# Kernel tuning notes

Measured on AMD Instinct MI355X. Metric: run time of the kernel, lower is better.

## Reference

```python
import jax, jax.numpy as jnp
import numpy as np

# ---- module config (mirrors arch_args / init_kwargs) ----
W_BITS_PER_SLICE = 4      # slice_init=True -> weights quantized with STE to w_bits_per_slice
A_BITS = 8                # activation quantization bits
A_BITS_PER_STREAM = 8
VMAX = 1.0
GON_HW, GOFF_HW = 1.0, 1e-3   # weight_to_diff_conductance is called with Gon=1, Goff=1/1000 (hardcoded)
ADC_PREC = 8
ADC_STEP = 1e-3           # adc_static_step
NUM_SUBARRAYS = 9
SUB_SIZE = 256            # subarray_size; 256*3*3 / 256 = 9 even chunks
K, STRIDE, PAD = 3, 1, 1


def ste_quantize(x, bits):
    # Symmetric uniform quantizer with straight-through estimator (STE_Quantize).
    n = float(2 ** bits - 1)
    s = jnp.max(jnp.abs(x)) + 1e-12
    q = jnp.round(x / s * n) / n * s
    return x + jax.lax.stop_gradient(q - x)


def adc_quantize(I):
    # Nbit_ADC: static-step uniform ADC, signed (adc_pos_only=False), deterministic
    # rounding (adc_stoch_round=False), STE backward, no custom loss.
    half = 2 ** (ADC_PREC - 1)
    q = jnp.clip(jnp.round(I / ADC_STEP), -half, half - 1) * ADC_STEP
    return I + jax.lax.stop_gradient(q - I)


def setup_inputs():
    key = jax.random.key(0)
    k1, k2 = jax.random.split(key)
    x = jax.random.normal(k1, (32, 256, 32, 32), jnp.float32)
    fan_in = 256 * K * K
    w = jax.random.normal(k2, (256, 256, K, K), jnp.float32) * np.sqrt(2.0 / fan_in)  # kaiming_normal
    return {"inputs": x, "weight": w}


def reference(inputs, weight):
    B = inputs.shape[0]
    O = weight.shape[0]

    # forward(): quantize activations (a_bits) and weights (w_bits_per_slice, slice_init path)
    qa = ste_quantize(inputs, A_BITS)
    qw = ste_quantize(weight, W_BITS_PER_SLICE)

    # F.unfold -> [B, C*k*k, L], channel-major patch ordering (matches torch)
    patches = jax.lax.conv_general_dilated_patches(
        qa, (K, K), (STRIDE, STRIDE), ((PAD, PAD), (PAD, PAD)))
    Hp, Wp = patches.shape[2], patches.shape[3]
    L = Hp * Wp
    V = patches.reshape(B, NUM_SUBARRAYS, SUB_SIZE, L) * (VMAX / A_BITS_PER_STREAM)

    # Differential conductances: G_pos - G_neg. The dummy columns (both filled with
    # Goff) cancel exactly in I_pos - I_neg, so the net current per subarray is a
    # single contraction against qw * (Gon - Goff) / Nstates_slice.
    nstates = float(2 ** W_BITS_PER_SLICE - 1)
    Gd = qw.reshape(O, NUM_SUBARRAYS, SUB_SIZE) * ((GON_HW - GOFF_HW) / nstates)

    # per-subarray crossbar currents: [B, n_sub, O, L]
    I = jnp.einsum('bgfl,ogf->bgol', V, Gd)

    # shared ADC applied to each subarray output, then accumulate over subarrays
    accum = adc_quantize(I).sum(axis=1)  # [B, O, L]
    a_loss = jnp.float32(0.0)            # adc_custom_loss=False

    # F.fold with (1,1) kernel onto sqrt(L) x sqrt(L) grid == reshape
    result = accum.reshape(B, O, Hp, Wp)
    return (result, a_loss)
```

## Files before the change

### kernel.cpp

```cpp
#include <hip/hip_runtime.h>
#include <stdint.h>

typedef unsigned short u16;
typedef __attribute__((ext_vector_type(8))) short short8;
typedef __attribute__((ext_vector_type(4))) float floatx4;

#define NB 32
#define NC 256
#define NH 32
#define NW 32
#define NO 256
#define NPIX (NH*NW)
#define KPIX 9
#define NG 9
#define RUN 32
#define GK (NG*RUN)
#define KTOT (NG*GK)
#define PADH 34
#define PADSP (PADH*PADH)
#define QA_BSTRIDE (PADSP*NC)

#define AS1 __attribute__((address_space(1)))
#define AS3 __attribute__((address_space(3)))

__global__ void fused_pre(const float4* __restrict__ x4, int nx4,
                          const float4* __restrict__ w4, int nw4,
                          float* __restrict__ pmax, u16* __restrict__ qa) {
  int bid = blockIdx.x;
  if (bid >= 1088) {
    int zb = bid - 1088;
    int b = zb / 9;
    int rem = (zb % 9) * 256 + threadIdx.x;
    if (rem >= 2112) return;
    int pb = rem >> 4, c16 = rem & 15;
    int y, x;
    if (pb < 68) { y = (pb >= 34) ? 33 : 0; x = pb % 34; }
    else { int q = pb - 68; y = 1 + (q >> 1); x = (q & 1) ? 33 : 0; }
    uint4 z; z.x = z.y = z.z = z.w = 0u;
    *(uint4*)(qa + ((size_t)(b * PADH + y) * PADH + x) * NC + c16 * 16) = z;
    return;
  }
  const float4* p; int n4; int nb, b0;
  if (bid < 1024) { p = x4; n4 = nx4; nb = 1024; b0 = bid; }
  else            { p = w4; n4 = nw4; nb = 64;   b0 = bid - 1024; }
  float m = 0.f;
  for (int i = b0 * blockDim.x + threadIdx.x; i < n4; i += nb * blockDim.x) {
    float4 v = p[i];
    m = fmaxf(m, fmaxf(fmaxf(fabsf(v.x), fabsf(v.y)), fmaxf(fabsf(v.z), fabsf(v.w))));
  }
#pragma unroll
  for (int off = 32; off > 0; off >>= 1)
    m = fmaxf(m, __shfl_down(m, off, 64));
  __shared__ float sm[4];
  int lane = threadIdx.x & 63, wv = threadIdx.x >> 6;
  if (lane == 0) sm[wv] = m;
  __syncthreads();
  if (threadIdx.x == 0)
    pmax[bid] = fmaxf(fmaxf(sm[0], sm[1]), fmaxf(sm[2], sm[3]));
}

__device__ inline void reduce_pmax(const float* pmax, int tid, int nthreads,
                                   float* sred, float& mx_out, float& mw_out) {
  const float4* pf4 = (const float4*)pmax;
  float mx = 0.f, mw = 0.f;
  for (int t = tid; t < 256; t += nthreads) {
    float4 v = pf4[t];
    mx = fmaxf(mx, fmaxf(fmaxf(v.x, v.y), fmaxf(v.z, v.w)));
  }
  if (tid < 16) {
    float4 v = pf4[256 + tid];
    mw = fmaxf(fmaxf(v.x, v.y), fmaxf(v.z, v.w));
  }
#pragma unroll
  for (int off = 32; off > 0; off >>= 1) {
    mx = fmaxf(mx, __shfl_down(mx, off, 64));
    mw = fmaxf(mw, __shfl_down(mw, off, 64));
  }
  int lane = tid & 63, wv = tid >> 6, nw = nthreads >> 6;
  if (lane == 0) { sred[wv] = mx; sred[8 + wv] = mw; }
  __syncthreads();
  mx = sred[0]; mw = sred[8];
  for (int i = 1; i < nw; i++) { mx = fmaxf(mx, sred[i]); mw = fmaxf(mw, sred[8 + i]); }
  mx_out = mx; mw_out = mw;
}

__global__ void fused_quant(const float* __restrict__ x, const float* __restrict__ w,
                            const float* __restrict__ pmax,
                            u16* __restrict__ qa, u16* __restrict__ wq,
                            float* __restrict__ lossp) {
  __shared__ float sred[16];
  float mx, mw;
  reduce_pmax(pmax, threadIdx.x, 256, sred, mx, mw);
  int bid = blockIdx.x, tid = threadIdx.x;
  if (bid < 1024) {
    __shared__ u16 ts[32][264];
    double s = (double)mx + 1e-12;
    double inv = 255.0 / s;
    int b = bid >> 5, y = bid & 31;
    const float4* x4 = (const float4*)x;
    int xc = tid & 7, crow = tid >> 3;
#pragma unroll
    for (int it = 0; it < 8; it++) {
      int c = crow + 32 * it;
      float4 v = x4[((size_t)(b * NC + c) * NH + y) * 8 + xc];
      float q0 = (float)rint((double)v.x * inv);
      float q1 = (float)rint((double)v.y * inv);
      float q2 = (float)rint((double)v.z * inv);
      float q3 = (float)rint((double)v.w * inv);
      ts[xc * 4 + 0][c] = (u16)(__float_as_uint(q0) >> 16);
      ts[xc * 4 + 1][c] = (u16)(__float_as_uint(q1) >> 16);
      ts[xc * 4 + 2][c] = (u16)(__float_as_uint(q2) >> 16);
      ts[xc * 4 + 3][c] = (u16)(__float_as_uint(q3) >> 16);
    }
    __syncthreads();
    int xx = tid >> 3, qwl = tid & 7;
    u16* orow = qa + ((size_t)(b * PADH + y + 1) * PADH + (xx + 1)) * NC;
#pragma unroll
    for (int it = 0; it < 4; it++) {
      int qw = qwl + 8 * it;
      *(uint4*)(orow + qw * 8) = *(const uint4*)&ts[xx][qw * 8];
    }
    return;
  }
  double s = (double)mw + 1e-12;
  double inv = 15.0 / s;
  int idx = (bid - 1024) * 256 + tid;
  if (idx == 0) *lossp = 0.0f;
  int o = idx / KTOT, kk = idx % KTOT;
  int g = kk / GK, rem = kk % GK;
  int r = rem / RUN, j = rem % RUN;
  int clo = (256 * g - r + 8) / 9;
  int chi = (256 * (g + 1) - r + 8) / 9; if (chi > NC) chi = NC;
  int cst = clo & ~3;
  int c = cst + j;
  float val = 0.f;
  if (c >= clo && c < chi) {
    float wv = w[((size_t)o * NC + c) * KPIX + r];
    val = (float)rint((double)wv * inv);
  }
  wq[idx] = (u16)(__float_as_uint(val) >> 16);
}

__global__ __launch_bounds__(256, 2) void gemm_adc(const u16* __restrict__ qa,
                                                   const u16* __restrict__ wq,
                                                   const float* __restrict__ pmax,
                                                   float* __restrict__ out) {
  __shared__ u16 lA[3 * 128 * RUN];
  __shared__ u16 lB[3 * 128 * RUN];
  __shared__ float sred[16];
  const int tid = threadIdx.x;
  float mx, mw;
  reduce_pmax(pmax, tid, 256, sred, mx, mw);

  const int mblk = blockIdx.x, nblk = blockIdx.y;
  const int b = mblk >> 3;
  const int p0 = (mblk & 7) * 128;
  const int n0 = nblk * 128;
  const int lane = tid & 63, wv = tid >> 6;
  const int wm = (wv & 1) * 64, wn = (wv >> 1) * 64;
  const int fm = lane & 15, fq = lane >> 4;
  const int swz = (fq + ((fm >> 1) & 3)) & 3;

  double sa = (double)mx + 1e-12;
  double sw = (double)mw + 1e-12;
  double Sstep = sa * sw * 0.999 / 459.0;

  const int r0 = tid >> 2;
  const int jsrc = ((tid & 3) - ((tid >> 3) & 3)) & 3;
  const u16* AbH[2]; const u16* BbH[2];
#pragma unroll
  for (int h = 0; h < 2; h++) {
    int row = r0 + 64 * h;
    int p = p0 + row;
    AbH[h] = qa + (size_t)b * QA_BSTRIDE
             + (((p >> 5) + 1) * PADH + ((p & 31) + 1)) * NC + jsrc * 8;
    BbH[h] = wq + (size_t)(n0 + row) * KTOT + jsrc * 8;
  }

  floatx4 acc[4][4];
  float tot[4][4][4];
#pragma unroll
  for (int mi = 0; mi < 4; mi++)
#pragma unroll
    for (int ni = 0; ni < 4; ni++)
#pragma unroll
      for (int rr = 0; rr < 4; rr++) { acc[mi][ni][rr] = 0.f; tot[mi][ni][rr] = 0.f; }

#pragma unroll 1
  for (int g = 0; g < NG; g++) {
#pragma unroll 1
    for (int rc = 0; rc < 3; rc++) {
      int offA[3], kb[3];
#pragma unroll
      for (int ri = 0; ri < 3; ri++) {
        int r = rc * 3 + ri;
        int cst = ((256 * g - r + 8) / 9) & ~3;
        offA[ri] = ((rc - 1) * PADH + (ri - 1)) * NC + cst;
        kb[ri] = g * GK + r * RUN;
      }
#pragma unroll
      for (int i = 0; i < 6; i++)
        __builtin_amdgcn_global_load_lds(
            (const AS1 void*)(AbH[i & 1] + offA[i >> 1]),
            (AS3 void*)&lA[(tid + 256 * i) * 8], 16, 0, 0);
#pragma unroll
      for (int i = 0; i < 6; i++)
        __builtin_amdgcn_global_load_lds(
            (const AS1 void*)(BbH[i & 1] + kb[i >> 1]),
            (AS3 void*)&lB[(tid + 256 * i) * 8], 16, 0, 0);
      __syncthreads();
#pragma unroll
      for (int ri = 0; ri < 3; ri++) {
        short8 afr[4], bfr[4];
#pragma unroll
        for (int mi = 0; mi < 4; mi++)
          afr[mi] = *(const short8*)&lA[ri * 4096 + (wm + mi * 16 + fm) * RUN + swz * 8];
#pragma unroll
        for (int ni = 0; ni < 4; ni++)
          bfr[ni] = *(const short8*)&lB[ri * 4096 + (wn + ni * 16 + fm) * RUN + swz * 8];
#pragma unroll
        for (int mi = 0; mi < 4; mi++)
#pragma unroll
          for (int ni = 0; ni < 4; ni++)
            acc[mi][ni] = __builtin_amdgcn_mfma_f32_16x16x32_bf16(afr[mi], bfr[ni], acc[mi][ni], 0, 0, 0);
      }
      __syncthreads();
    }
#pragma unroll
    for (int mi = 0; mi < 4; mi++)
#pragma unroll
      for (int ni = 0; ni < 4; ni++)
#pragma unroll
        for (int rr = 0; rr < 4; rr++) {
          double d = (double)acc[mi][ni][rr] * Sstep;
          float tf = (float)rint(d);
          tf = fminf(fmaxf(tf, -128.f), 127.f);
          tot[mi][ni][rr] += tf;
          acc[mi][ni][rr] = 0.f;
        }
  }
#pragma unroll
  for (int mi = 0; mi < 4; mi++)
#pragma unroll
    for (int ni = 0; ni < 4; ni++) {
      int o = n0 + wn + ni * 16 + fm;
      int p = p0 + wm + mi * 16 + fq * 4;
      float4 o4;
      o4.x = tot[mi][ni][0] * 1e-3f;
      o4.y = tot[mi][ni][1] * 1e-3f;
      o4.z = tot[mi][ni][2] * 1e-3f;
      o4.w = tot[mi][ni][3] * 1e-3f;
      *(float4*)(out + ((size_t)(b * NO + o)) * NPIX + p) = o4;
    }
}

extern "C" void kernel_launch(void* const* d_in, const int* in_sizes, int n_in,
                              void* d_out, int out_size, void* d_ws, size_t ws_size,
                              hipStream_t stream) {
  const float* x = (const float*)d_in[0];
  const float* w = (const float*)d_in[1];
  float* out = (float*)d_out;

  float* pmax = (float*)d_ws;
  u16* qa = (u16*)((char*)d_ws + 8192);
  u16* wq = (u16*)((char*)d_ws + 8192 + 18939904 + 8192);

  fused_pre<<<1376, 256, 0, stream>>>((const float4*)x, (NB * NC * NH * NW) / 4,
                                      (const float4*)w, (NO * NC * KPIX) / 4,
                                      pmax, qa);
  fused_quant<<<1024 + 2592, 256, 0, stream>>>(x, w, pmax, qa, wq, out + (out_size - 1));
  gemm_adc<<<dim3(256, 2), 256, 0, stream>>>(qa, wq, pmax, out);
}
```

Baseline: 158.6 us.

## Double-buffer LDS loads in gemm_adc and enlarge block tile to 256x128

The GEMM+ADC kernel now uses 512 threads per block with a 256-pixel by 128-output tile, so each B tile is shared across twice as many rows. Global-to-LDS loads are double-buffered: the next stage is issued before computing the current one, with a partial vmcnt wait and raw barriers replacing __syncthreads, and MFMA sections run at raised wave priority. This aims to hide load latency and cut redundant weight traffic. The cost is a larger LDS footprint (about 144KB per block), which may limit occupancy to one block per CU, and only 256 blocks in the grid.

```diff
diff --git a/kernel.cpp b/kernel.cpp
--- a/kernel.cpp
+++ b/kernel.cpp
@@ -141,23 +141,23 @@
   wq[idx] = (u16)(__float_as_uint(val) >> 16);
 }
 
-__global__ __launch_bounds__(256, 2) void gemm_adc(const u16* __restrict__ qa,
+__global__ __launch_bounds__(512, 2) void gemm_adc(const u16* __restrict__ qa,
                                                    const u16* __restrict__ wq,
                                                    const float* __restrict__ pmax,
                                                    float* __restrict__ out) {
-  __shared__ u16 lA[3 * 128 * RUN];
-  __shared__ u16 lB[3 * 128 * RUN];
+  __shared__ u16 lA[2 * 3 * 256 * RUN];
+  __shared__ u16 lB[2 * 3 * 128 * RUN];
   __shared__ float sred[16];
   const int tid = threadIdx.x;
   float mx, mw;
-  reduce_pmax(pmax, tid, 256, sred, mx, mw);
+  reduce_pmax(pmax, tid, 512, sred, mx, mw);
 
   const int mblk = blockIdx.x, nblk = blockIdx.y;
-  const int b = mblk >> 3;
-  const int p0 = (mblk & 7) * 128;
+  const int b = mblk >> 2;
+  const int p0 = (mblk & 3) * 256;
   const int n0 = nblk * 128;
   const int lane = tid & 63, wv = tid >> 6;
-  const int wm = (wv & 1) * 64, wn = (wv >> 1) * 64;
+  const int wm = (wv & 3) * 64, wn = (wv >> 2) * 64;
   const int fm = lane & 15, fq = lane >> 4;
   const int swz = (fq + ((fm >> 1) & 3)) & 3;
 
@@ -167,15 +167,14 @@
 
   const int r0 = tid >> 2;
   const int jsrc = ((tid & 3) - ((tid >> 3) & 3)) & 3;
-  const u16* AbH[2]; const u16* BbH[2];
+  const u16* AbH[2];
 #pragma unroll
   for (int h = 0; h < 2; h++) {
-    int row = r0 + 64 * h;
-    int p = p0 + row;
+    int p = p0 + r0 + 128 * h;
     AbH[h] = qa + (size_t)b * QA_BSTRIDE
              + (((p >> 5) + 1) * PADH + ((p & 31) + 1)) * NC + jsrc * 8;
-    BbH[h] = wq + (size_t)(n0 + row) * KTOT + jsrc * 8;
-  }
+  }
+  const u16* Bb = wq + (size_t)(n0 + r0) * KTOT + jsrc * 8;
 
   floatx4 acc[4][4];
   float tot[4][4][4];
@@ -186,46 +185,28 @@
 #pragma unroll
       for (int rr = 0; rr < 4; rr++) { acc[mi][ni][rr] = 0.f; tot[mi][ni][rr] = 0.f; }
 
-#pragma unroll 1
-  for (int g = 0; g < NG; g++) {
-#pragma unroll 1
-    for (int rc = 0; rc < 3; rc++) {
-      int offA[3], kb[3];
-#pragma unroll
-      for (int ri = 0; ri < 3; ri++) {
-        int r = rc * 3 + ri;
-        int cst = ((256 * g - r + 8) / 9) & ~3;
-        offA[ri] = ((rc - 1) * PADH + (ri - 1)) * NC + cst;
-        kb[ri] = g * GK + r * RUN;
-      }
-#pragma unroll
-      for (int i = 0; i < 6; i++)
-        __builtin_amdgcn_global_load_lds(
-            (const AS1 void*)(AbH[i & 1] + offA[i >> 1]),
-            (AS3 void*)&lA[(tid + 256 * i) * 8], 16, 0, 0);
-#pragma unroll
-      for (int i = 0; i < 6; i++)
-        __builtin_amdgcn_global_load_lds(
-            (const AS1 void*)(BbH[i & 1] + kb[i >> 1]),
-            (AS3 void*)&lB[(tid + 256 * i) * 8], 16, 0, 0);
-      __syncthreads();
-#pragma unroll
-      for (int ri = 0; ri < 3; ri++) {
-        short8 afr[4], bfr[4];
-#pragma unroll
-        for (int mi = 0; mi < 4; mi++)
-          afr[mi] = *(const short8*)&lA[ri * 4096 + (wm + mi * 16 + fm) * RUN + swz * 8];
-#pragma unroll
-        for (int ni = 0; ni < 4; ni++)
-          bfr[ni] = *(const short8*)&lB[ri * 4096 + (wn + ni * 16 + fm) * RUN + swz * 8];
-#pragma unroll
-        for (int mi = 0; mi < 4; mi++)
-#pragma unroll
-          for (int ni = 0; ni < 4; ni++)
-            acc[mi][ni] = __builtin_amdgcn_mfma_f32_16x16x32_bf16(afr[mi], bfr[ni], acc[mi][ni], 0, 0, 0);
-      }
-      __syncthreads();
-    }
+  auto STAGE = [&](int gs, int rcs, int aB, int bB) {
+    int offA[3], kb[3];
+#pragma unroll
+    for (int ri = 0; ri < 3; ri++) {
+      int r = rcs * 3 + ri;
+      int cst = ((256 * gs - r + 8) / 9) & ~3;
+      offA[ri] = ((rcs - 1) * PADH + (ri - 1)) * NC + cst;
+      kb[ri] = gs * GK + r * RUN;
+    }
+#pragma unroll
+    for (int i = 0; i < 6; i++)
+      __builtin_amdgcn_global_load_lds(
+          (const AS1 void*)(AbH[i & 1] + offA[i >> 1]),
+          (AS3 void*)&lA[aB + i * 4096 + tid * 8], 16, 0, 0);
+#pragma unroll
+    for (int i = 0; i < 3; i++)
+      __builtin_amdgcn_global_load_lds(
+          (const AS1 void*)(Bb + kb[i]),
+          (AS3 void*)&lB[bB + i * 4096 + tid * 8], 16, 0, 0);
+  };
+
+  auto FOLD = [&]() {
 #pragma unroll
     for (int mi = 0; mi < 4; mi++)
 #pragma unroll
@@ -238,7 +219,46 @@
           tot[mi][ni][rr] += tf;
           acc[mi][ni][rr] = 0.f;
         }
-  }
+  };
+
+  STAGE(0, 0, 0, 0);
+  int gs = 0, rcs = 1;
+
+#pragma unroll 1
+  for (int t = 0; t < 27; ++t) {
+    const int aB = (t & 1) * 24576, bB = (t & 1) * 12288;
+    if (t < 26) {
+      STAGE(gs, rcs, aB ^ 24576, bB ^ 12288);
+      if (++rcs == 3) { rcs = 0; ++gs; }
+    }
+    if (t > 0 && (t % 3) == 0) FOLD();
+    if (t < 26) { asm volatile("s_waitcnt vmcnt(9)" ::: "memory"); }
+    else        { asm volatile("s_waitcnt vmcnt(0)" ::: "memory"); }
+    __builtin_amdgcn_s_barrier();
+    asm volatile("" ::: "memory");
+    __builtin_amdgcn_s_setprio(1);
+#pragma unroll
+    for (int ri = 0; ri < 3; ri++) {
+      short8 afr[4], bfr[4];
+#pragma unroll
+      for (int mi = 0; mi < 4; mi++)
+        afr[mi] = *(const short8*)&lA[aB + ri * 8192 + (wm + mi * 16 + fm) * RUN + swz * 8];
+#pragma unroll
+      for (int ni = 0; ni < 4; ni++)
+        bfr[ni] = *(const short8*)&lB[bB + ri * 4096 + (wn + ni * 16 + fm) * RUN + swz * 8];
+#pragma unroll
+      for (int mi = 0; mi < 4; mi++)
+#pragma unroll
+        for (int ni = 0; ni < 4; ni++)
+          acc[mi][ni] = __builtin_amdgcn_mfma_f32_16x16x32_bf16(afr[mi], bfr[ni], acc[mi][ni], 0, 0, 0);
+    }
+    __builtin_amdgcn_s_setprio(0);
+    asm volatile("" ::: "memory");
+    __builtin_amdgcn_s_barrier();
+    asm volatile("" ::: "memory");
+  }
+  FOLD();
+
 #pragma unroll
   for (int mi = 0; mi < 4; mi++)
 #pragma unroll
@@ -269,5 +289,5 @@
                                       (const float4*)w, (NO * NC * KPIX) / 4,
                                       pmax, qa);
   fused_quant<<<1024 + 2592, 256, 0, stream>>>(x, w, pmax, qa, wq, out + (out_size - 1));
-  gemm_adc<<<dim3(256, 2), 256, 0, stream>>>(qa, wq, pmax, out);
-}
+  gemm_adc<<<dim3(128, 2), 512, 0, stream>>>(qa, wq, pmax, out);
+}
```

New measurement: 165.2 us. +4.2%, slower.

## Stage padded activation halo tile once per group and reuse across taps

Applied to the files above, without the earlier changes.

Instead of loading a separate 128x32 activation slice into LDS for each of the nine kernel taps, the GEMM loads a 6x34-pixel halo tile with 40 channels once per subarray group. It then reads the shifted windows for every tap directly from that tile. This cuts global-to-LDS traffic for the A operand by roughly half or more and drops the per-tap A loads in later rc iterations. In exchange, LDS reads lose the swizzle, so bank conflicts are possible, and unaligned channel offsets need split 8-byte loads.

```diff
diff --git a/kernel.cpp b/kernel.cpp
--- a/kernel.cpp
+++ b/kernel.cpp
@@ -3,6 +3,7 @@
 
 typedef unsigned short u16;
 typedef __attribute__((ext_vector_type(8))) short short8;
+typedef __attribute__((ext_vector_type(4))) short s4v;
 typedef __attribute__((ext_vector_type(4))) float floatx4;
 
 #define NB 32
@@ -19,6 +20,7 @@
 #define PADH 34
 #define PADSP (PADH*PADH)
 #define QA_BSTRIDE (PADSP*NC)
+#define CHS 40
 
 #define AS1 __attribute__((address_space(1)))
 #define AS3 __attribute__((address_space(3)))
@@ -145,7 +147,7 @@
                                                    const u16* __restrict__ wq,
                                                    const float* __restrict__ pmax,
                                                    float* __restrict__ out) {
-  __shared__ u16 lA[3 * 128 * RUN];
+  __shared__ u16 sA[8192];
   __shared__ u16 lB[3 * 128 * RUN];
   __shared__ float sred[16];
   const int tid = threadIdx.x;
@@ -155,27 +157,33 @@
   const int mblk = blockIdx.x, nblk = blockIdx.y;
   const int b = mblk >> 3;
   const int p0 = (mblk & 7) * 128;
+  const int y0 = (mblk & 7) * 4;
   const int n0 = nblk * 128;
   const int lane = tid & 63, wv = tid >> 6;
   const int wm = (wv & 1) * 64, wn = (wv >> 1) * 64;
   const int fm = lane & 15, fq = lane >> 4;
   const int swz = (fq + ((fm >> 1) & 3)) & 3;
+  const int fq8 = fq * 8;
 
   double sa = (double)mx + 1e-12;
   double sw = (double)mw + 1e-12;
   double Sstep = sa * sw * 0.999 / 459.0;
 
+  int pix40[4];
+#pragma unroll
+  for (int mi = 0; mi < 4; mi++) {
+    int pr = wm + mi * 16 + fm;
+    pix40[mi] = ((pr >> 5) * 34 + (pr & 31)) * CHS;
+  }
+
   const int r0 = tid >> 2;
   const int jsrc = ((tid & 3) - ((tid >> 3) & 3)) & 3;
-  const u16* AbH[2]; const u16* BbH[2];
-#pragma unroll
-  for (int h = 0; h < 2; h++) {
-    int row = r0 + 64 * h;
-    int p = p0 + row;
-    AbH[h] = qa + (size_t)b * QA_BSTRIDE
-             + (((p >> 5) + 1) * PADH + ((p & 31) + 1)) * NC + jsrc * 8;
-    BbH[h] = wq + (size_t)(n0 + row) * KTOT + jsrc * 8;
-  }
+  const u16* BbH[2];
+#pragma unroll
+  for (int h = 0; h < 2; h++)
+    BbH[h] = wq + (size_t)(n0 + r0 + 64 * h) * KTOT + jsrc * 8;
+
+  const u16* Abase = qa + (size_t)b * QA_BSTRIDE + (size_t)y0 * PADH * NC;
 
   floatx4 acc[4][4];
   float tot[4][4][4];
@@ -188,21 +196,31 @@
 
 #pragma unroll 1
   for (int g = 0; g < NG; g++) {
+    int cw = ((256 * g) / 9) & ~3;
 #pragma unroll 1
     for (int rc = 0; rc < 3; rc++) {
-      int offA[3], kb[3];
+      int kb[3], dA[3];
 #pragma unroll
       for (int ri = 0; ri < 3; ri++) {
         int r = rc * 3 + ri;
         int cst = ((256 * g - r + 8) / 9) & ~3;
-        offA[ri] = ((rc - 1) * PADH + (ri - 1)) * NC + cst;
+        dA[ri] = cst - cw;
         kb[ri] = g * GK + r * RUN;
       }
-#pragma unroll
-      for (int i = 0; i < 6; i++)
-        __builtin_amdgcn_global_load_lds(
-            (const AS1 void*)(AbH[i & 1] + offA[i >> 1]),
-            (AS3 void*)&lA[(tid + 256 * i) * 8], 16, 0, 0);
+      if (rc == 0) {
+        const u16* src = Abase + cw;
+#pragma unroll
+        for (int i = 0; i < 4; i++) {
+          int s = tid + 256 * i;
+          int py = s / 170;
+          int rem = s - py * 170;
+          int px = rem / 5;
+          int j = rem - px * 5;
+          __builtin_amdgcn_global_load_lds(
+              (const AS1 void*)(src + (py * PADH + px) * NC + j * 8),
+              (AS3 void*)&sA[s * 8], 16, 0, 0);
+        }
+      }
 #pragma unroll
       for (int i = 0; i < 6; i++)
         __builtin_amdgcn_global_load_lds(
@@ -212,9 +230,20 @@
 #pragma unroll
       for (int ri = 0; ri < 3; ri++) {
         short8 afr[4], bfr[4];
-#pragma unroll
-        for (int mi = 0; mi < 4; mi++)
-          afr[mi] = *(const short8*)&lA[ri * 4096 + (wm + mi * 16 + fm) * RUN + swz * 8];
+        int po = rc * (34 * CHS) + ri * CHS + dA[ri] + fq8;
+        if (dA[ri] == 0) {
+#pragma unroll
+          for (int mi = 0; mi < 4; mi++)
+            afr[mi] = *(const short8*)&sA[pix40[mi] + po];
+        } else {
+#pragma unroll
+          for (int mi = 0; mi < 4; mi++) {
+            union { short8 v8; s4v v4[2]; } u;
+            u.v4[0] = *(const s4v*)&sA[pix40[mi] + po];
+            u.v4[1] = *(const s4v*)&sA[pix40[mi] + po + 4];
+            afr[mi] = u.v8;
+          }
+        }
 #pragma unroll
         for (int ni = 0; ni < 4; ni++)
           bfr[ni] = *(const short8*)&lB[ri * 4096 + (wn + ni * 16 + fm) * RUN + swz * 8];
```

Measured after the change: 154.8 us. 2.4% less time.
